# Kernel tuning notes

Measured on AMD Instinct MI355X. Metric: run time of the kernel, lower is better.

## Reference

```python
import jax, jax.numpy as jnp
import numpy as np
import math

B, C_IN, C_OUT, W, H = 16, 64, 64, 256, 128
KW = 7  # conv kernel (1, 7), valid padding -> H' = H - 6


def _conv(x, w, b):
    # NCHW input, OIHW weight, valid padding, stride 1 (matches nn.Conv2d)
    y = jax.lax.conv_general_dilated(x, w, (1, 1), 'VALID',
                                     dimension_numbers=('NCHW', 'OIHW', 'NCHW'))
    return y + b[None, :, None, None]


def setup_inputs() -> dict:
    key = jax.random.key(0)
    ks = jax.random.split(key, 7)
    scale = 1.0 / math.sqrt(C_IN * KW)
    x = jax.random.normal(ks[0], (B, C_IN, W, H), jnp.float32)
    wK = jax.random.normal(ks[1], (C_OUT, C_IN, 1, KW), jnp.float32) * scale
    bK = jax.random.normal(ks[2], (C_OUT,), jnp.float32) * scale
    wQ = jax.random.normal(ks[3], (C_OUT, C_IN, 1, KW), jnp.float32) * scale
    bQ = jax.random.normal(ks[4], (C_OUT,), jnp.float32) * scale
    wV = jax.random.normal(ks[5], (C_OUT, C_IN, 1, KW), jnp.float32) * scale
    bV = jax.random.normal(ks[6], (C_OUT,), jnp.float32) * scale
    return {'x': x, 'wK': wK, 'bK': bK, 'wQ': wQ, 'bQ': bQ, 'wV': wV, 'bV': bV}


def reference(x, wK, bK, wQ, bQ, wV, bV):
    b, c, w, h = x.shape
    # raw row-major flatten of NCHW conv output into (B, W, C*H') -- faithful
    # to torch's .reshape(nbatches, w, -1) on a contiguous tensor
    k = _conv(x, wK, bK).reshape(b, w, -1)   # [B, W, C_OUT*(H-6)]
    q = _conv(x, wQ, bQ).reshape(b, w, -1)   # [B, W, C_OUT*(H-6)]
    v = x.reshape(b, w, -1)                  # [B, W, C_IN*H]
    d_k = q.shape[-1]
    scores = jnp.einsum('bqd,bkd->bqk', q, k) / math.sqrt(d_k)  # [B, W, W]
    i = jnp.arange(w)[:, None]
    j = jnp.arange(w)[None, :]
    blocked = ((i < 128) & (j < 128)) | ((i >= 128) & (j >= 128))
    scores = jnp.where(blocked, -jnp.inf, scores)
    p = jax.nn.softmax(scores, axis=-1)
    x1 = jnp.einsum('bqk,bkd->bqd', p, v).reshape(b, c, w, h)
    y = _conv(x1 + x, wV, bV)                # [B, C_OUT, W, H-6]
    return jnp.where(y >= 0, y, 0.2 * y)     # LeakyReLU(0.2)
```

## Files before the change

kernel.cpp:

```cpp
#include <hip/hip_runtime.h>
#include <hip/hip_bf16.h>

using uint32 = unsigned int;
using u16 = unsigned short;
using short8 = __attribute__((ext_vector_type(8))) short;
using f32x4  = __attribute__((ext_vector_type(4))) float;

__device__ __forceinline__ float bf2f(u16 u) {
  union { uint32 i; float f; } c; c.i = ((uint32)u) << 16; return c.f;
}
__device__ __forceinline__ u16 f2bf(float f) {
  union { float f; uint32 i; } c; c.f = f;
  uint32 u = c.i;
  u += 0x7fffu + ((u >> 16) & 1u);
  return (u16)(u >> 16);
}
__device__ __forceinline__ uint32 pack2(float a, float b) {
  return (uint32)f2bf(a) | ((uint32)f2bf(b) << 16);
}


__global__ __launch_bounds__(256) void prep_weights(
    const float* __restrict__ wK, const float* __restrict__ wQ,
    const float* __restrict__ wV,
    u16* __restrict__ pK, u16* __restrict__ pQ, u16* __restrict__ pV)
{
  int idx = blockIdx.x * 256 + threadIdx.x;
  if (idx >= 86016) return;
  int set = idx / 28672;
  int r = idx - set * 28672;
  int kw = r >> 12;
  int rem = r & 4095;
  int co = rem >> 6, ci = rem & 63;
  const float* src = set == 0 ? wK : (set == 1 ? wQ : wV);
  u16* dst = set == 0 ? pK : (set == 1 ? pQ : pV);
  dst[r] = f2bf(src[co * 448 + ci * 7 + kw]);
}

__global__ __launch_bounds__(256) void conv_kq_mfma(
    const float* __restrict__ x,
    const u16* __restrict__ wpK, const u16* __restrict__ wpQ,
    const float* __restrict__ bK, const float* __restrict__ bQ,
    u16* __restrict__ qbuf, u16* __restrict__ kbuf)
{
  __shared__ u16 xt[136 * 64];
  __shared__ u16 wlK[64 * 64];
  __shared__ u16 wlQ[64 * 64];
  const int bid = blockIdx.x;
  const int b = bid >> 8, w = bid & 255;
  const int t = threadIdx.x;
  const int lane = t & 63, wv = t >> 6;

  {
    const float* xb = x + (size_t)b * 2097152 + (size_t)w * 128;
    #pragma unroll
    for (int it = 0; it < 8; ++it) {
      int idx = t + it * 256;
      int h = idx & 127, g = idx >> 7;
      int ci0 = g * 4;
      float v0 = xb[(size_t)(ci0 + 0) * 32768 + h];
      float v1 = xb[(size_t)(ci0 + 1) * 32768 + h];
      float v2 = xb[(size_t)(ci0 + 2) * 32768 + h];
      float v3 = xb[(size_t)(ci0 + 3) * 32768 + h];
      uint2 pk;
      pk.x = pack2(v0, v1);
      pk.y = pack2(v2, v3);
      int col = ci0 ^ ((h & 7) << 3);
      *reinterpret_cast<uint2*>(&xt[h * 64 + col]) = pk;
    }
    if (t < 128) {
      int h = 128 + (t >> 4), g = t & 15;
      *reinterpret_cast<uint2*>(&xt[h * 64 + g * 4]) = make_uint2(0u, 0u);
    }
  }

  f32x4 accK[4][2], accQ[4][2];
  #pragma unroll
  for (int mt = 0; mt < 4; ++mt)
    #pragma unroll
    for (int j = 0; j < 2; ++j) {
      accK[mt][j] = (f32x4)0.f;
      accQ[mt][j] = (f32x4)0.f;
    }

  for (int kw = 0; kw < 7; ++kw) {
    __syncthreads();
    #pragma unroll
    for (int it = 0; it < 4; ++it) {
      int idx = t + it * 256;
      int co = idx >> 4, q = idx & 15;
      int ci0 = q * 4;
      int col = ci0 ^ ((co & 7) << 3);
      uint2 dk = *reinterpret_cast<const uint2*>(wpK + ((size_t)(kw * 64 + co) * 64 + ci0));
      uint2 dq = *reinterpret_cast<const uint2*>(wpQ + ((size_t)(kw * 64 + co) * 64 + ci0));
      *reinterpret_cast<uint2*>(&wlK[co * 64 + col]) = dk;
      *reinterpret_cast<uint2*>(&wlQ[co * 64 + col]) = dq;
    }
    __syncthreads();
    #pragma unroll
    for (int ks = 0; ks < 2; ++ks) {
      int cib = ks * 32 + ((lane >> 4) << 3);
      short8 bfr[2];
      #pragma unroll
      for (int j = 0; j < 2; ++j) {
        int row = (wv * 2 + j) * 16 + (lane & 15) + kw;
        int col = cib ^ ((row & 7) << 3);
        bfr[j] = *reinterpret_cast<const short8*>(&xt[row * 64 + col]);
      }
      #pragma unroll
      for (int mt = 0; mt < 4; ++mt) {
        int co = mt * 16 + (lane & 15);
        int col = cib ^ ((co & 7) << 3);
        short8 aK = *reinterpret_cast<const short8*>(&wlK[co * 64 + col]);
        short8 aQ = *reinterpret_cast<const short8*>(&wlQ[co * 64 + col]);
        #pragma unroll
        for (int j = 0; j < 2; ++j) {
          accK[mt][j] = __builtin_amdgcn_mfma_f32_16x16x32_bf16(aK, bfr[j], accK[mt][j], 0, 0, 0);
          accQ[mt][j] = __builtin_amdgcn_mfma_f32_16x16x32_bf16(aQ, bfr[j], accQ[mt][j], 0, 0, 0);
        }
      }
    }
  }

  #pragma unroll
  for (int mt = 0; mt < 4; ++mt) {
    #pragma unroll
    for (int r = 0; r < 4; ++r) {
      int co = mt * 16 + (lane >> 4) * 4 + r;
      float bk = bK[co], bq = bQ[co];
      size_t base = ((size_t)(b * 64 + co) * 256 + w) * 122;
      #pragma unroll
      for (int j = 0; j < 2; ++j) {
        int n = (wv * 2 + j) * 16 + (lane & 15);
        if (n < 122) {
          kbuf[base + n] = f2bf(accK[mt][j][r] + bk);
          qbuf[base + n] = f2bf(accQ[mt][j][r] + bq);
        }
      }
    }
  }
}

__global__ __launch_bounds__(256) void scores_mfma(
    const u16* __restrict__ qbuf, const u16* __restrict__ kbuf,
    float* __restrict__ pbuf)
{
  __shared__ float lmax[4][16];
  __shared__ float lsum[4][16];
  const int bid = blockIdx.x;
  const int b = bid & 15, rt = bid >> 4;
  const int t = threadIdx.x;
  const int lane = t & 63, wq = t >> 6;
  const int g = lane >> 4, ln = lane & 15;
  const int i0 = rt * 16;
  const int jbase = (rt < 8) ? 128 : 0;

  const u16* qp  = qbuf + (size_t)(b * 256 + i0 + ln) * 7808 + g * 8;
  const u16* kp0 = kbuf + (size_t)(b * 256 + jbase + wq * 32 + ln) * 7808 + g * 8;
  const u16* kp1 = kp0 + (size_t)16 * 7808;

  f32x4 acc0 = (f32x4)0.f, acc1 = (f32x4)0.f;
  #pragma unroll 4
  for (int c = 0; c < 244; ++c) {
    short8 af = *reinterpret_cast<const short8*>(qp + c * 32);
    short8 b0 = *reinterpret_cast<const short8*>(kp0 + c * 32);
    short8 b1 = *reinterpret_cast<const short8*>(kp1 + c * 32);
    acc0 = __builtin_amdgcn_mfma_f32_16x16x32_bf16(af, b0, acc0, 0, 0, 0);
    acc1 = __builtin_amdgcn_mfma_f32_16x16x32_bf16(af, b1, acc1, 0, 0, 0);
  }

  const float scale = 0.011316967f;
  float s0[4], s1[4];
  #pragma unroll
  for (int r = 0; r < 4; ++r) { s0[r] = acc0[r] * scale; s1[r] = acc1[r] * scale; }

  float pm[4], ps[4];
  #pragma unroll
  for (int r = 0; r < 4; ++r) {
    float m = fmaxf(s0[r], s1[r]);
    #pragma unroll
    for (int off = 8; off >= 1; off >>= 1) m = fmaxf(m, __shfl_xor(m, off));
    float e = __expf(s0[r] - m) + __expf(s1[r] - m);
    #pragma unroll
    for (int off = 8; off >= 1; off >>= 1) e += __shfl_xor(e, off);
    pm[r] = m; ps[r] = e;
  }
  if (ln == 0) {
    #pragma unroll
    for (int r = 0; r < 4; ++r) {
      lmax[wq][g * 4 + r] = pm[r];
      lsum[wq][g * 4 + r] = ps[r];
    }
  }
  __syncthreads();

  #pragma unroll
  for (int r = 0; r < 4; ++r) {
    int row = g * 4 + r;
    float m0 = lmax[0][row], m1 = lmax[1][row], m2 = lmax[2][row], m3 = lmax[3][row];
    float mm = fmaxf(fmaxf(m0, m1), fmaxf(m2, m3));
    float ss = lsum[0][row] * __expf(m0 - mm) + lsum[1][row] * __expf(m1 - mm)
             + lsum[2][row] * __expf(m2 - mm) + lsum[3][row] * __expf(m3 - mm);
    float inv = 1.0f / ss;
    float p0 = __expf(s0[r] - mm) * inv;
    float p1 = __expf(s1[r] - mm) * inv;
    float* prow = pbuf + (size_t)(b * 256 + i0 + row) * 128 + wq * 32 + ln;
    prow[0]  = p0;
    prow[16] = p1;
  }
}

__global__ __launch_bounds__(256) void pv_mfma(
    const float* __restrict__ pbuf, const float* __restrict__ x,
    u16* __restrict__ zbuf)
{
  __shared__ u16 pl[128 * 136];
  __shared__ u16 vt[256 * 40];
  const int bid = blockIdx.x;
  const int b  = bid >> 6;
  const int hb = (bid >> 5) & 1;
  const int ec = bid & 31;
  const int t = threadIdx.x;
  const int lane = t & 63, wv = t >> 6;
  const int ln = lane & 15, g = lane >> 4;

  const int i0 = hb ? 0 : 128;
  const int jbase = hb ? 128 : 0;
  const int e0 = ec * 256;
  const float* xb = x + (size_t)b * 2097152;
  const float* pb = pbuf + (size_t)(b * 256 + i0) * 128;

  uint32* plw = reinterpret_cast<uint32*>(pl);
  #pragma unroll
  for (int it = 0; it < 32; ++it) {
    int idx = t + it * 256;
    int ii = idx >> 6, jjp = idx & 63;
    float2 f2 = *reinterpret_cast<const float2*>(pb + ii * 128 + jjp * 2);
    plw[ii * 68 + jjp] = pack2(f2.x, f2.y);
  }

  f32x4 acc[2][16];
  #pragma unroll
  for (int mt = 0; mt < 2; ++mt)
    #pragma unroll
    for (int nt = 0; nt < 16; ++nt) acc[mt][nt] = (f32x4)0.f;

  uint32* vtw = reinterpret_cast<uint32*>(vt);
  for (int ks = 0; ks < 4; ++ks) {
    __syncthreads();
    #pragma unroll
    for (int it = 0; it < 16; ++it) {
      int idx = t + it * 256;
      int e = idx & 255, jp = idx >> 8;
      const float* vr = xb + (size_t)(jbase + ks * 32 + jp * 2) * 8192 + e0 + e;
      float f0 = vr[0];
      float f1 = vr[8192];
      vtw[e * 20 + jp] = pack2(f0, f1);
    }
    __syncthreads();
    short8 af[2];
    #pragma unroll
    for (int mt = 0; mt < 2; ++mt) {
      int row = wv * 32 + mt * 16 + ln;
      af[mt] = *reinterpret_cast<const short8*>(&pl[row * 136 + ks * 32 + g * 8]);
    }
    #pragma unroll
    for (int nt = 0; nt < 16; ++nt) {
      int e = nt * 16 + ln;
      short8 bf = *reinterpret_cast<const short8*>(&vt[e * 40 + g * 8]);
      acc[0][nt] = __builtin_amdgcn_mfma_f32_16x16x32_bf16(af[0], bf, acc[0][nt], 0, 0, 0);
      acc[1][nt] = __builtin_amdgcn_mfma_f32_16x16x32_bf16(af[1], bf, acc[1][nt], 0, 0, 0);
    }
  }

  #pragma unroll
  for (int mt = 0; mt < 2; ++mt) {
    #pragma unroll
    for (int r = 0; r < 4; ++r) {
      int i = i0 + wv * 32 + mt * 16 + g * 4 + r;
      const float* xr = xb + (size_t)i * 8192 + e0 + ln;
      u16* zr = zbuf + (size_t)(b * 256 + i) * 8192 + e0 + ln;
      #pragma unroll
      for (int nt = 0; nt < 16; ++nt) {
        float z = xr[nt * 16] + acc[mt][nt][r];
        zr[nt * 16] = f2bf(z);
      }
    }
  }
}

__global__ __launch_bounds__(256) void conv_out_mfma(
    const u16* __restrict__ zbuf, const u16* __restrict__ wpV,
    const float* __restrict__ bV, float* __restrict__ out)
{
  __shared__ u16 xt[136 * 64];
  __shared__ u16 wl[64 * 64];
  const int bid = blockIdx.x;
  const int b = bid >> 8, w = bid & 255;
  const int t = threadIdx.x;
  const int lane = t & 63, wv = t >> 6;

  {
    const u16* zb = zbuf + (size_t)b * 2097152 + (size_t)w * 128;
    #pragma unroll
    for (int it = 0; it < 8; ++it) {
      int idx = t + it * 256;
      int h = idx & 127, g = idx >> 7;
      int ci0 = g * 4;
      u16 v0 = zb[(size_t)(ci0 + 0) * 32768 + h];
      u16 v1 = zb[(size_t)(ci0 + 1) * 32768 + h];
      u16 v2 = zb[(size_t)(ci0 + 2) * 32768 + h];
      u16 v3 = zb[(size_t)(ci0 + 3) * 32768 + h];
      uint2 pk;
      pk.x = (uint32)v0 | ((uint32)v1 << 16);
      pk.y = (uint32)v2 | ((uint32)v3 << 16);
      int col = ci0 ^ ((h & 7) << 3);
      *reinterpret_cast<uint2*>(&xt[h * 64 + col]) = pk;
    }
    if (t < 128) {
      int h = 128 + (t >> 4), g = t & 15;
      *reinterpret_cast<uint2*>(&xt[h * 64 + g * 4]) = make_uint2(0u, 0u);
    }
  }

  f32x4 acc[4][2];
  #pragma unroll
  for (int mt = 0; mt < 4; ++mt)
    #pragma unroll
    for (int j = 0; j < 2; ++j) acc[mt][j] = (f32x4)0.f;

  for (int kw = 0; kw < 7; ++kw) {
    __syncthreads();
    #pragma unroll
    for (int it = 0; it < 4; ++it) {
      int idx = t + it * 256;
      int co = idx >> 4, q = idx & 15;
      int ci0 = q * 4;
      int col = ci0 ^ ((co & 7) << 3);
      uint2 d = *reinterpret_cast<const uint2*>(wpV + ((size_t)(kw * 64 + co) * 64 + ci0));
      *reinterpret_cast<uint2*>(&wl[co * 64 + col]) = d;
    }
    __syncthreads();
    #pragma unroll
    for (int ks = 0; ks < 2; ++ks) {
      int cib = ks * 32 + ((lane >> 4) << 3);
      short8 bfr[2];
      #pragma unroll
      for (int j = 0; j < 2; ++j) {
        int row = (wv * 2 + j) * 16 + (lane & 15) + kw;
        int col = cib ^ ((row & 7) << 3);
        bfr[j] = *reinterpret_cast<const short8*>(&xt[row * 64 + col]);
      }
      #pragma unroll
      for (int mt = 0; mt < 4; ++mt) {
        int co = mt * 16 + (lane & 15);
        int col = cib ^ ((co & 7) << 3);
        short8 aV = *reinterpret_cast<const short8*>(&wl[co * 64 + col]);
        #pragma unroll
        for (int j = 0; j < 2; ++j)
          acc[mt][j] = __builtin_amdgcn_mfma_f32_16x16x32_bf16(aV, bfr[j], acc[mt][j], 0, 0, 0);
      }
    }
  }

  #pragma unroll
  for (int mt = 0; mt < 4; ++mt) {
    #pragma unroll
    for (int r = 0; r < 4; ++r) {
      int co = mt * 16 + (lane >> 4) * 4 + r;
      float bv = bV[co];
      size_t base = ((size_t)(b * 64 + co) * 256 + w) * 122;
      #pragma unroll
      for (int j = 0; j < 2; ++j) {
        int n = (wv * 2 + j) * 16 + (lane & 15);
        if (n < 122) {
          float y = acc[mt][j][r] + bv;
          out[base + n] = (y >= 0.f) ? y : 0.2f * y;
        }
      }
    }
  }
}

extern "C" void kernel_launch(void* const* d_in, const int* in_sizes, int n_in,
                              void* d_out, int out_size, void* d_ws, size_t ws_size,
                              hipStream_t stream) {
  const float* x  = (const float*)d_in[0];
  const float* wK = (const float*)d_in[1];
  const float* bK = (const float*)d_in[2];
  const float* wQ = (const float*)d_in[3];
  const float* bQ = (const float*)d_in[4];
  const float* wV = (const float*)d_in[5];
  const float* bV = (const float*)d_in[6];
  float* out = (float*)d_out;

  char* ws = (char*)d_ws;
  u16* qbuf  = (u16*)ws;
  u16* zbuf  = (u16*)ws;
  u16* kbuf  = (u16*)(ws + 67108864);
  float* pbuf = (float*)(ws + 131072000);
  u16* wpK = (u16*)(ws + 133169152);
  u16* wpQ = (u16*)(ws + 133226496);
  u16* wpV = (u16*)(ws + 133283840);

  prep_weights<<<dim3(336), dim3(256), 0, stream>>>(wK, wQ, wV, wpK, wpQ, wpV);
  conv_kq_mfma<<<dim3(16 * 256), dim3(256), 0, stream>>>(x, wpK, wpQ, bK, bQ, qbuf, kbuf);
  scores_mfma<<<dim3(256), dim3(256), 0, stream>>>(qbuf, kbuf, pbuf);
  pv_mfma<<<dim3(1024), dim3(256), 0, stream>>>(pbuf, x, zbuf);
  conv_out_mfma<<<dim3(16 * 256), dim3(256), 0, stream>>>(zbuf, wpV, bV, out);
}
```

Before: 336.0 us.

## Read conv weights directly from global into registers, remap waves to output-channel tiles

Both conv kernels stop staging per-kw weight slices in LDS. Each wave now owns a 16-output-channel tile and loads its A fragments straight from global memory, which L2 serves because every block reads the same weights. This removes 14 block-wide barriers per block and the LDS weight traffic, and cuts LDS use so more blocks fit per CU. In exchange each wave reads all 8 position tiles of x from LDS, so LDS reads of the input go up, and weight loads become global-latency bound.

```diff
diff --git a/kernel.cpp b/kernel.cpp
--- a/kernel.cpp
+++ b/kernel.cpp
@@ -44,20 +44,19 @@
     u16* __restrict__ qbuf, u16* __restrict__ kbuf)
 {
   __shared__ u16 xt[136 * 64];
-  __shared__ u16 wlK[64 * 64];
-  __shared__ u16 wlQ[64 * 64];
   const int bid = blockIdx.x;
   const int b = bid >> 8, w = bid & 255;
   const int t = threadIdx.x;
   const int lane = t & 63, wv = t >> 6;
+  const int ln = lane & 15, g = lane >> 4;
 
   {
     const float* xb = x + (size_t)b * 2097152 + (size_t)w * 128;
     #pragma unroll
     for (int it = 0; it < 8; ++it) {
       int idx = t + it * 256;
-      int h = idx & 127, g = idx >> 7;
-      int ci0 = g * 4;
+      int h = idx & 127, gq = idx >> 7;
+      int ci0 = gq * 4;
       float v0 = xb[(size_t)(ci0 + 0) * 32768 + h];
       float v1 = xb[(size_t)(ci0 + 1) * 32768 + h];
       float v2 = xb[(size_t)(ci0 + 2) * 32768 + h];
@@ -69,73 +68,45 @@
       *reinterpret_cast<uint2*>(&xt[h * 64 + col]) = pk;
     }
     if (t < 128) {
-      int h = 128 + (t >> 4), g = t & 15;
-      *reinterpret_cast<uint2*>(&xt[h * 64 + g * 4]) = make_uint2(0u, 0u);
-    }
-  }
-
-  f32x4 accK[4][2], accQ[4][2];
-  #pragma unroll
-  for (int mt = 0; mt < 4; ++mt)
-    #pragma unroll
-    for (int j = 0; j < 2; ++j) {
-      accK[mt][j] = (f32x4)0.f;
-      accQ[mt][j] = (f32x4)0.f;
-    }
+      int h = 128 + (t >> 4), gq = t & 15;
+      *reinterpret_cast<uint2*>(&xt[h * 64 + gq * 4]) = make_uint2(0u, 0u);
+    }
+  }
+  __syncthreads();
+
+  f32x4 accK[8], accQ[8];
+  #pragma unroll
+  for (int j = 0; j < 8; ++j) { accK[j] = (f32x4)0.f; accQ[j] = (f32x4)0.f; }
 
   for (int kw = 0; kw < 7; ++kw) {
-    __syncthreads();
-    #pragma unroll
-    for (int it = 0; it < 4; ++it) {
-      int idx = t + it * 256;
-      int co = idx >> 4, q = idx & 15;
-      int ci0 = q * 4;
-      int col = ci0 ^ ((co & 7) << 3);
-      uint2 dk = *reinterpret_cast<const uint2*>(wpK + ((size_t)(kw * 64 + co) * 64 + ci0));
-      uint2 dq = *reinterpret_cast<const uint2*>(wpQ + ((size_t)(kw * 64 + co) * 64 + ci0));
-      *reinterpret_cast<uint2*>(&wlK[co * 64 + col]) = dk;
-      *reinterpret_cast<uint2*>(&wlQ[co * 64 + col]) = dq;
-    }
-    __syncthreads();
     #pragma unroll
     for (int ks = 0; ks < 2; ++ks) {
-      int cib = ks * 32 + ((lane >> 4) << 3);
-      short8 bfr[2];
+      const int kb = ks * 32 + g * 8;
+      const size_t woff = (size_t)(kw * 64 + wv * 16 + ln) * 64 + kb;
+      short8 aK = *reinterpret_cast<const short8*>(wpK + woff);
+      short8 aQ = *reinterpret_cast<const short8*>(wpQ + woff);
       #pragma unroll
-      for (int j = 0; j < 2; ++j) {
-        int row = (wv * 2 + j) * 16 + (lane & 15) + kw;
-        int col = cib ^ ((row & 7) << 3);
-        bfr[j] = *reinterpret_cast<const short8*>(&xt[row * 64 + col]);
-      }
-      #pragma unroll
-      for (int mt = 0; mt < 4; ++mt) {
-        int co = mt * 16 + (lane & 15);
-        int col = cib ^ ((co & 7) << 3);
-        short8 aK = *reinterpret_cast<const short8*>(&wlK[co * 64 + col]);
-        short8 aQ = *reinterpret_cast<const short8*>(&wlQ[co * 64 + col]);
-        #pragma unroll
-        for (int j = 0; j < 2; ++j) {
-          accK[mt][j] = __builtin_amdgcn_mfma_f32_16x16x32_bf16(aK, bfr[j], accK[mt][j], 0, 0, 0);
-          accQ[mt][j] = __builtin_amdgcn_mfma_f32_16x16x32_bf16(aQ, bfr[j], accQ[mt][j], 0, 0, 0);
-        }
-      }
-    }
-  }
-
-  #pragma unroll
-  for (int mt = 0; mt < 4; ++mt) {
-    #pragma unroll
-    for (int r = 0; r < 4; ++r) {
-      int co = mt * 16 + (lane >> 4) * 4 + r;
-      float bk = bK[co], bq = bQ[co];
-      size_t base = ((size_t)(b * 64 + co) * 256 + w) * 122;
-      #pragma unroll
-      for (int j = 0; j < 2; ++j) {
-        int n = (wv * 2 + j) * 16 + (lane & 15);
-        if (n < 122) {
-          kbuf[base + n] = f2bf(accK[mt][j][r] + bk);
-          qbuf[base + n] = f2bf(accQ[mt][j][r] + bq);
-        }
+      for (int j = 0; j < 8; ++j) {
+        int row = j * 16 + ln + kw;
+        int col = kb ^ ((row & 7) << 3);
+        short8 bf = *reinterpret_cast<const short8*>(&xt[row * 64 + col]);
+        accK[j] = __builtin_amdgcn_mfma_f32_16x16x32_bf16(aK, bf, accK[j], 0, 0, 0);
+        accQ[j] = __builtin_amdgcn_mfma_f32_16x16x32_bf16(aQ, bf, accQ[j], 0, 0, 0);
+      }
+    }
+  }
+
+  #pragma unroll
+  for (int r = 0; r < 4; ++r) {
+    int co = wv * 16 + g * 4 + r;
+    float bk = bK[co], bq = bQ[co];
+    size_t base = ((size_t)(b * 64 + co) * 256 + w) * 122;
+    #pragma unroll
+    for (int j = 0; j < 8; ++j) {
+      int n = j * 16 + ln;
+      if (n < 122) {
+        kbuf[base + n] = f2bf(accK[j][r] + bk);
+        qbuf[base + n] = f2bf(accQ[j][r] + bq);
       }
     }
   }
@@ -294,19 +265,19 @@
     const float* __restrict__ bV, float* __restrict__ out)
 {
   __shared__ u16 xt[136 * 64];
-  __shared__ u16 wl[64 * 64];
   const int bid = blockIdx.x;
   const int b = bid >> 8, w = bid & 255;
   const int t = threadIdx.x;
   const int lane = t & 63, wv = t >> 6;
+  const int ln = lane & 15, g = lane >> 4;
 
   {
     const u16* zb = zbuf + (size_t)b * 2097152 + (size_t)w * 128;
     #pragma unroll
     for (int it = 0; it < 8; ++it) {
       int idx = t + it * 256;
-      int h = idx & 127, g = idx >> 7;
-      int ci0 = g * 4;
+      int h = idx & 127, gq = idx >> 7;
+      int ci0 = gq * 4;
       u16 v0 = zb[(size_t)(ci0 + 0) * 32768 + h];
       u16 v1 = zb[(size_t)(ci0 + 1) * 32768 + h];
       u16 v2 = zb[(size_t)(ci0 + 2) * 32768 + h];
@@ -318,65 +289,43 @@
       *reinterpret_cast<uint2*>(&xt[h * 64 + col]) = pk;
     }
     if (t < 128) {
-      int h = 128 + (t >> 4), g = t & 15;
-      *reinterpret_cast<uint2*>(&xt[h * 64 + g * 4]) = make_uint2(0u, 0u);
-    }
-  }
-
-  f32x4 acc[4][2];
-  #pragma unroll
-  for (int mt = 0; mt < 4; ++mt)
-    #pragma unroll
-    for (int j = 0; j < 2; ++j) acc[mt][j] = (f32x4)0.f;
+      int h = 128 + (t >> 4), gq = t & 15;
+      *reinterpret_cast<uint2*>(&xt[h * 64 + gq * 4]) = make_uint2(0u, 0u);
+    }
+  }
+  __syncthreads();
+
+  f32x4 acc[8];
+  #pragma unroll
+  for (int j = 0; j < 8; ++j) acc[j] = (f32x4)0.f;
 
   for (int kw = 0; kw < 7; ++kw) {
-    __syncthreads();
-    #pragma unroll
-    for (int it = 0; it < 4; ++it) {
-      int idx = t + it * 256;
-      int co = idx >> 4, q = idx & 15;
-      int ci0 = q * 4;
-      int col = ci0 ^ ((co & 7) << 3);
-      uint2 d = *reinterpret_cast<const uint2*>(wpV + ((size_t)(kw * 64 + co) * 64 + ci0));
-      *reinterpret_cast<uint2*>(&wl[co * 64 + col]) = d;
-    }
-    __syncthreads();
     #pragma unroll
     for (int ks = 0; ks < 2; ++ks) {
-      int cib = ks * 32 + ((lane >> 4) << 3);
-      short8 bfr[2];
+      const int kb = ks * 32 + g * 8;
+      const size_t woff = (size_t)(kw * 64 + wv * 16 + ln) * 64 + kb;
+      short8 aV = *reinterpret_cast<const short8*>(wpV + woff);
       #pragma unroll
-      for (int j = 0; j < 2; ++j) {
-        int row = (wv * 2 + j) * 16 + (lane & 15) + kw;
-        int col = cib ^ ((row & 7) << 3);
-        bfr[j] = *reinterpret_cast<const short8*>(&xt[row * 64 + col]);
-      }
-      #pragma unroll
-      for (int mt = 0; mt < 4; ++mt) {
-        int co = mt * 16 + (lane & 15);
-        int col = cib ^ ((co & 7) << 3);
-        short8 aV = *reinterpret_cast<const short8*>(&wl[co * 64 + col]);
-        #pragma unroll
-        for (int j = 0; j < 2; ++j)
-          acc[mt][j] = __builtin_amdgcn_mfma_f32_16x16x32_bf16(aV, bfr[j], acc[mt][j], 0, 0, 0);
-      }
-    }
-  }
-
-  #pragma unroll
-  for (int mt = 0; mt < 4; ++mt) {
-    #pragma unroll
-    for (int r = 0; r < 4; ++r) {
-      int co = mt * 16 + (lane >> 4) * 4 + r;
-      float bv = bV[co];
-      size_t base = ((size_t)(b * 64 + co) * 256 + w) * 122;
-      #pragma unroll
-      for (int j = 0; j < 2; ++j) {
-        int n = (wv * 2 + j) * 16 + (lane & 15);
-        if (n < 122) {
-          float y = acc[mt][j][r] + bv;
-          out[base + n] = (y >= 0.f) ? y : 0.2f * y;
-        }
+      for (int j = 0; j < 8; ++j) {
+        int row = j * 16 + ln + kw;
+        int col = kb ^ ((row & 7) << 3);
+        short8 bf = *reinterpret_cast<const short8*>(&xt[row * 64 + col]);
+        acc[j] = __builtin_amdgcn_mfma_f32_16x16x32_bf16(aV, bf, acc[j], 0, 0, 0);
+      }
+    }
+  }
+
+  #pragma unroll
+  for (int r = 0; r < 4; ++r) {
+    int co = wv * 16 + g * 4 + r;
+    float bv = bV[co];
+    size_t base = ((size_t)(b * 64 + co) * 256 + w) * 122;
+    #pragma unroll
+    for (int j = 0; j < 8; ++j) {
+      int n = j * 16 + ln;
+      if (n < 122) {
+        float y = acc[j][r] + bv;
+        out[base + n] = (y >= 0.f) ? y : 0.2f * y;
       }
     }
   }
```

New measurement: 342.6 us. About the same (+2.0%).
